# Kernel optimization log

Measured on AMD Instinct MI355X. Metric: run time of the kernel, lower is better.

The kernel has to match this reference:

```python
import jax, jax.numpy as jnp
import numpy as np

EMBED_DIM = 1024
NUM_HEADS = 16
HEAD_DIM = EMBED_DIM // NUM_HEADS


def setup_inputs() -> dict:
    key = jax.random.key(0)
    ks = jax.random.split(key, 9)
    B, S, E = 4, 2048, EMBED_DIM
    scale = 1.0 / np.sqrt(E)
    x = jax.random.normal(ks[0], (B, S, E), dtype=jnp.float32)
    # Linear layers: weight [E, E] (out, in) and bias [E], torch-style init scale
    Wq = jax.random.uniform(ks[1], (E, E), jnp.float32, -scale, scale)
    bq = jax.random.uniform(ks[2], (E,), jnp.float32, -scale, scale)
    Wk = jax.random.uniform(ks[3], (E, E), jnp.float32, -scale, scale)
    bk = jax.random.uniform(ks[4], (E,), jnp.float32, -scale, scale)
    Wv = jax.random.uniform(ks[5], (E, E), jnp.float32, -scale, scale)
    bv = jax.random.uniform(ks[6], (E,), jnp.float32, -scale, scale)
    Wo = jax.random.uniform(ks[7], (E, E), jnp.float32, -scale, scale)
    bo = jax.random.uniform(ks[8], (E,), jnp.float32, -scale, scale)
    return {"x": x, "Wq": Wq, "bq": bq, "Wk": Wk, "bk": bk,
            "Wv": Wv, "bv": bv, "Wo": Wo, "bo": bo}


def reference(x, Wq, bq, Wk, bk, Wv, bv, Wo, bo):
    B, S, E = x.shape
    H, D = NUM_HEADS, HEAD_DIM

    def proj(W, b):
        # torch Linear: x @ W.T + b ; reshape to [B, H, S, D]
        y = jnp.einsum('bse,fe->bsf', x, W) + b
        return y.reshape(B, S, H, D).transpose(0, 2, 1, 3)

    Q = proj(Wq, bq)
    K = proj(Wk, bk)
    V = proj(Wv, bv)
    scores = jnp.einsum('bhqd,bhkd->bhqk', Q, K) / jnp.sqrt(
        jnp.asarray(D, dtype=jnp.float32))
    attn = jax.nn.softmax(scores, axis=-1)
    out = jnp.einsum('bhqk,bhkd->bhqd', attn, V)
    out = out.transpose(0, 2, 1, 3).reshape(B, S, E)
    out = jnp.einsum('bse,fe->bsf', out, Wo) + bo
    return out
```

## Files before the change

### kernel.cpp

```cpp
#include <hip/hip_runtime.h>
#include <math.h>

#define SEQ 2048
#define EMB 1024
#define NH 16
#define HD 64
#define BATCH 4
#define MROWS (BATCH * SEQ)

typedef unsigned short u16;
typedef unsigned int u32;
typedef _Float16 f16;
using half8   = __attribute__((ext_vector_type(8))) f16;
using fp16x2  = __attribute__((ext_vector_type(2))) __fp16;
using vfloat4 = __attribute__((ext_vector_type(4))) float;

__device__ __forceinline__ u16 f2h(float f) {
    union { f16 h; u16 u; } x; x.h = (f16)f; return x.u;
}
__device__ __forceinline__ u32 pk2h(float a, float b) {
    union { fp16x2 h; u32 u; } x;
    x.h = __builtin_amdgcn_cvt_pkrtz(a, b);
    return x.u;
}
__device__ __forceinline__ float exp2v(float x) {
    float r; asm("v_exp_f32 %0, %1" : "=v"(r) : "v"(x)); return r;
}

__device__ __forceinline__ void gload16(const void* g, void* l) {
    __builtin_amdgcn_global_load_lds(
        (const __attribute__((address_space(1))) void*)g,
        (__attribute__((address_space(3))) void*)l, 16, 0, 0);
}

__global__ __launch_bounds__(256) void cvt5_kernel(
    const float* __restrict__ x,  const float* __restrict__ wq,
    const float* __restrict__ wk, const float* __restrict__ wv,
    const float* __restrict__ wo,
    uint2* __restrict__ xh, uint2* __restrict__ wqkv, uint2* __restrict__ woh)
{
    int gid = blockIdx.x * 256 + threadIdx.x;
    const float4* src; uint2* dst; int o;
    if (gid < (1 << 21)) {
        src = (const float4*)x; dst = xh; o = gid;
    } else {
        int g = gid - (1 << 21);
        int r = g >> 18;
        o = g & ((1 << 18) - 1);
        if      (r == 0) { src = (const float4*)wq; dst = wqkv; }
        else if (r == 1) { src = (const float4*)wk; dst = wqkv + (1 << 18); }
        else if (r == 2) { src = (const float4*)wv; dst = wqkv + (2 << 18); }
        else             { src = (const float4*)wo; dst = woh; }
    }
    float4 v = src[o];
    dst[o] = make_uint2(pk2h(v.x, v.y), pk2h(v.z, v.w));
}

__global__ __launch_bounds__(256) void gemm_qkv_kernel(
    const u16* __restrict__ A, const u16* __restrict__ Wqkv,
    const float* __restrict__ bq, const float* __restrict__ bk,
    const float* __restrict__ bv,
    u16* __restrict__ Qo, u16* __restrict__ Ko, u16* __restrict__ Vo,
    float sq)
{
    __shared__ char lds[32768];
    const int tid = threadIdx.x, wave = tid >> 6, lane = tid & 63;
    const int swz = (blockIdx.x & 7) * 192 + (blockIdx.x >> 3);
    const int bn = swz % 24, bm = swz / 24;
    const int mat = bn >> 3;
    const int wr = wave >> 1, wc = wave & 1;

    const int srow  = wave * 16 + (lane >> 2);
    const int sslot = lane & 3;
    const int ldso  = wave * 1024 + (lane << 4);
    const u16* Ab = A    + (size_t)bm * 128 * EMB;
    const u16* Wb = Wqkv + (size_t)bn * 128 * EMB;

    vfloat4 acc[4][4] = {};

#define QKV_STAGE(k0, bufi)                                                   \
    {                                                                         \
        char* Ad = lds + (bufi) * 16384;                                      \
        char* Bd = Ad + 8192;                                                 \
        _Pragma("unroll")                                                     \
        for (int i2 = 0; i2 < 2; ++i2) {                                      \
            int row = i2 * 64 + srow;                                         \
            int ko  = ((sslot ^ ((row >> 1) & 3)) << 3);                      \
            gload16(Ab + (size_t)row * EMB + (k0) + ko, Ad + i2 * 4096 + ldso); \
            gload16(Wb + (size_t)row * EMB + (k0) + ko, Bd + i2 * 4096 + ldso); \
        }                                                                     \
    }

    QKV_STAGE(0, 0);
    __syncthreads();

    for (int it = 0; it < EMB / 32; ++it) {
        const int cur = it & 1;
        if (it + 1 < EMB / 32) QKV_STAGE((it + 1) * 32, cur ^ 1);

        char* As = lds + cur * 16384;
        char* Bs = As + 8192;
        half8 af[4], bfr[4];
        #pragma unroll
        for (int m = 0; m < 4; ++m) {
            int r = wr * 64 + m * 16 + (lane & 15);
            af[m] = *(const half8*)(As + r * 64 + ((((lane >> 4) ^ ((r >> 1) & 3)) << 4)));
        }
        #pragma unroll
        for (int n = 0; n < 4; ++n) {
            int r = wc * 64 + n * 16 + (lane & 15);
            bfr[n] = *(const half8*)(Bs + r * 64 + ((((lane >> 4) ^ ((r >> 1) & 3)) << 4)));
        }
        #pragma unroll
        for (int m = 0; m < 4; ++m)
            #pragma unroll
            for (int n = 0; n < 4; ++n)
                acc[m][n] = __builtin_amdgcn_mfma_f32_16x16x32_f16(af[m], bfr[n], acc[m][n], 0, 0, 0);

        __syncthreads();
    }
#undef QKV_STAGE

    const float* bp = (mat == 0) ? bq : ((mat == 1) ? bk : bv);
    const float scale = (mat == 0) ? sq : 1.0f;
    u16* Co = (mat == 0) ? Qo : ((mat == 1) ? Ko : Vo);
    const int row0 = bm * 128 + wr * 64;
    const int col0 = (bn & 7) * 128 + wc * 64;

    #pragma unroll
    for (int n = 0; n < 4; ++n) {
        int col = col0 + n * 16 + (lane & 15);
        float bb = bp[col];
        int h = col >> 6, d = col & 63;
        if (mat != 2) {
            #pragma unroll
            for (int m = 0; m < 4; ++m)
                #pragma unroll
                for (int j = 0; j < 4; ++j) {
                    int row = row0 + m * 16 + (lane >> 4) * 4 + j;
                    int b = row >> 11, s = row & (SEQ - 1);
                    Co[(((size_t)(b * NH + h)) * SEQ + s) * HD + d] =
                        f2h((acc[m][n][j] + bb) * scale);
                }
        } else {
            #pragma unroll
            for (int m = 0; m < 4; ++m) {
                int row = row0 + m * 16 + (lane >> 4) * 4;
                int b = row >> 11, s = row & (SEQ - 1);
                u32 w0 = pk2h(acc[m][n][0] + bb, acc[m][n][1] + bb);
                u32 w1 = pk2h(acc[m][n][2] + bb, acc[m][n][3] + bb);
                *(uint2*)(Co + (((size_t)(b * NH + h)) * HD + d) * SEQ + s) =
                    make_uint2(w0, w1);
            }
        }
    }
}

__global__ __launch_bounds__(256) void gemm_f16_kernel(
    const u16* __restrict__ A, const u16* __restrict__ W,
    const float* __restrict__ bias, float* __restrict__ C)
{
    __shared__ char lds[32768];
    const int tid = threadIdx.x, wave = tid >> 6, lane = tid & 63;
    const int swz = (blockIdx.x & 7) * 64 + (blockIdx.x >> 3);
    const int bn = swz & 7, bm = swz >> 3;
    const int wr = wave >> 1, wc = wave & 1;

    const int srow  = wave * 16 + (lane >> 2);
    const int sslot = lane & 3;
    const int ldso  = wave * 1024 + (lane << 4);
    const u16* Ab = A + (size_t)bm * 128 * EMB;
    const u16* Wb = W + (size_t)bn * 128 * EMB;

    vfloat4 acc[4][4] = {};

#define F16_STAGE(k0, bufi)                                                   \
    {                                                                         \
        char* Ad = lds + (bufi) * 16384;                                      \
        char* Bd = Ad + 8192;                                                 \
        _Pragma("unroll")                                                     \
        for (int i2 = 0; i2 < 2; ++i2) {                                      \
            int row = i2 * 64 + srow;                                         \
            int ko  = ((sslot ^ ((row >> 1) & 3)) << 3);                      \
            gload16(Ab + (size_t)row * EMB + (k0) + ko, Ad + i2 * 4096 + ldso); \
            gload16(Wb + (size_t)row * EMB + (k0) + ko, Bd + i2 * 4096 + ldso); \
        }                                                                     \
    }

    F16_STAGE(0, 0);
    __syncthreads();

    for (int it = 0; it < EMB / 32; ++it) {
        const int cur = it & 1;
        if (it + 1 < EMB / 32) F16_STAGE((it + 1) * 32, cur ^ 1);

        char* As = lds + cur * 16384;
        char* Bs = As + 8192;
        half8 af[4], bfr[4];
        #pragma unroll
        for (int m = 0; m < 4; ++m) {
            int r = wr * 64 + m * 16 + (lane & 15);
            af[m] = *(const half8*)(As + r * 64 + ((((lane >> 4) ^ ((r >> 1) & 3)) << 4)));
        }
        #pragma unroll
        for (int n = 0; n < 4; ++n) {
            int r = wc * 64 + n * 16 + (lane & 15);
            bfr[n] = *(const half8*)(Bs + r * 64 + ((((lane >> 4) ^ ((r >> 1) & 3)) << 4)));
        }
        #pragma unroll
        for (int m = 0; m < 4; ++m)
            #pragma unroll
            for (int n = 0; n < 4; ++n)
                acc[m][n] = __builtin_amdgcn_mfma_f32_16x16x32_f16(af[m], bfr[n], acc[m][n], 0, 0, 0);

        __syncthreads();
    }
#undef F16_STAGE

    const int row0 = bm * 128 + wr * 64, col0 = bn * 128 + wc * 64;
    #pragma unroll
    for (int n = 0; n < 4; ++n) {
        int col = col0 + n * 16 + (lane & 15);
        float bb = bias[col];
        #pragma unroll
        for (int m = 0; m < 4; ++m)
            #pragma unroll
            for (int j = 0; j < 4; ++j) {
                int row = row0 + m * 16 + (lane >> 4) * 4 + j;
                C[(size_t)row * EMB + col] = acc[m][n][j] + bb;
            }
    }
}

__device__ __forceinline__ void stage_rows(const u16* g, int rstride, char* dst,
                                           int wave, int lane) {
    int r = wave * 8 + (lane >> 3), sl = lane & 7;
    #pragma unroll
    for (int i2 = 0; i2 < 2; ++i2) {
        int row = i2 * 32 + r;
        gload16(g + (size_t)row * rstride + ((sl ^ (row & 7)) << 3),
                dst + i2 * 4096 + wave * 1024 + (lane << 4));
    }
}

__global__ __launch_bounds__(256) void attn_kernel(
    const u16* __restrict__ Q, const u16* __restrict__ K,
    const u16* __restrict__ Vt, u16* __restrict__ O)
{
    __shared__ char lds[40960];
    char* QPs = lds;
    char* Kb0 = lds + 8192;
    char* Kb1 = lds + 16384;
    char* Vb0 = lds + 24576;
    char* Vb1 = lds + 32768;

    const int tid = threadIdx.x, wave = tid >> 6, lane = tid & 63;
    const int c = lane >> 4, li = lane & 15;

    const int swz = (blockIdx.x & 7) * 128 + (blockIdx.x >> 3);
    const int bh = swz >> 4;
    const int q0 = (swz & 15) << 7;

    const u16* Qg = Q  + ((size_t)bh * SEQ + q0) * HD;
    const u16* Kg = K  + (size_t)bh * SEQ * HD;
    const u16* Vg = Vt + (size_t)bh * HD * SEQ;

    const int srow8 = wave * 8 + (lane >> 3);
    const int ssl   = lane & 7;
    const int swzo  = ((ssl ^ (srow8 & 7)) << 3);
    const int ldo   = wave * 1024 + (lane << 4);
    const u16* kp = Kg + (size_t)srow8 * HD + swzo;
    const u16* vp = Vg + (size_t)srow8 * SEQ + swzo;

    stage_rows(Qg, HD, QPs, wave, lane);
    gload16(kp, Kb0 + ldo);  gload16(kp + 32 * HD, Kb0 + 4096 + ldo);
    gload16(vp, Vb0 + ldo);  gload16(vp + 32 * SEQ, Vb0 + 4096 + ldo);
    kp += 64 * HD;  vp += 64;
    __syncthreads();

    half8 qf[2][2];
    const int q = wave * 16 + li;
    #pragma unroll
    for (int cc = 0; cc < 2; ++cc)
        qf[0][cc] = *(const half8*)(QPs + q * 128 + (((4 * cc + c) ^ (q & 7)) << 4));
    __syncthreads();
    stage_rows(Qg + (size_t)64 * HD, HD, QPs, wave, lane);
    __syncthreads();
    #pragma unroll
    for (int cc = 0; cc < 2; ++cc)
        qf[1][cc] = *(const half8*)(QPs + q * 128 + (((4 * cc + c) ^ (q & 7)) << 4));

    const half8 ones8 = {1, 1, 1, 1, 1, 1, 1, 1};
    char* Pw = QPs + wave * 2048;
    vfloat4 o0[4] = {}, o1[4] = {};
    vfloat4 l0 = {}, l1 = {};

    for (int kt = 0; kt < SEQ / 64; ++kt) {
        char* Kc = (kt & 1) ? Kb1 : Kb0;
        char* Vc = (kt & 1) ? Vb1 : Vb0;
        if (kt < SEQ / 64 - 1) {
            char* kd = (kt & 1) ? Kb0 : Kb1;
            char* vd = (kt & 1) ? Vb0 : Vb1;
            gload16(kp, kd + ldo);  gload16(kp + 32 * HD, kd + 4096 + ldo);
            gload16(vp, vd + ldo);  gload16(vp + 32 * SEQ, vd + 4096 + ldo);
            kp += 64 * HD;  vp += 64;
        }

        vfloat4 s0[4] = {}, s1[4] = {};
        __builtin_amdgcn_s_setprio(1);
        #pragma unroll
        for (int n = 0; n < 4; ++n) {
            int key = 16 * n + li;
            #pragma unroll
            for (int cc = 0; cc < 2; ++cc) {
                half8 kb = *(const half8*)(Kc + key * 128 + (((4 * cc + c) ^ (li & 7)) << 4));
                s0[n] = __builtin_amdgcn_mfma_f32_16x16x32_f16(kb, qf[0][cc], s0[n], 0, 0, 0);
                s1[n] = __builtin_amdgcn_mfma_f32_16x16x32_f16(kb, qf[1][cc], s1[n], 0, 0, 0);
            }
        }
        __builtin_amdgcn_s_setprio(0);

        #pragma unroll
        for (int n = 0; n < 4; ++n)
            #pragma unroll
            for (int j = 0; j < 4; ++j) {
                s0[n][j] = exp2v(s0[n][j]);
                s1[n][j] = exp2v(s1[n][j]);
            }

        half8 pf0[2], pf1[2];
        #pragma unroll
        for (int n = 0; n < 4; ++n) {
            u32 w0 = pk2h(s0[n][0], s0[n][1]);
            u32 w1 = pk2h(s0[n][2], s0[n][3]);
            *(uint2*)(Pw + li * 128 + (((2 * n + (c >> 1)) ^ (li & 7)) << 4) + ((c & 1) << 3))
                = make_uint2(w0, w1);
        }
        #pragma unroll
        for (int cc = 0; cc < 2; ++cc)
            pf0[cc] = *(const half8*)(Pw + li * 128 + (((4 * cc + c) ^ (li & 7)) << 4));
        #pragma unroll
        for (int n = 0; n < 4; ++n) {
            u32 w0 = pk2h(s1[n][0], s1[n][1]);
            u32 w1 = pk2h(s1[n][2], s1[n][3]);
            *(uint2*)(Pw + li * 128 + (((2 * n + (c >> 1)) ^ (li & 7)) << 4) + ((c & 1) << 3))
                = make_uint2(w0, w1);
        }
        #pragma unroll
        for (int cc = 0; cc < 2; ++cc)
            pf1[cc] = *(const half8*)(Pw + li * 128 + (((4 * cc + c) ^ (li & 7)) << 4));

        __builtin_amdgcn_s_setprio(1);
        #pragma unroll
        for (int n = 0; n < 4; ++n) {
            int r = 16 * n + li;
            #pragma unroll
            for (int cc = 0; cc < 2; ++cc) {
                half8 vf = *(const half8*)(Vc + r * 128 + (((4 * cc + c) ^ (li & 7)) << 4));
                o0[n] = __builtin_amdgcn_mfma_f32_16x16x32_f16(vf, pf0[cc], o0[n], 0, 0, 0);
                o1[n] = __builtin_amdgcn_mfma_f32_16x16x32_f16(vf, pf1[cc], o1[n], 0, 0, 0);
            }
        }
        #pragma unroll
        for (int cc = 0; cc < 2; ++cc) {
            l0 = __builtin_amdgcn_mfma_f32_16x16x32_f16(ones8, pf0[cc], l0, 0, 0, 0);
            l1 = __builtin_amdgcn_mfma_f32_16x16x32_f16(ones8, pf1[cc], l1, 0, 0, 0);
        }
        __builtin_amdgcn_s_setprio(0);

        __syncthreads();
    }

    const int b = bh >> 4, h = bh & 15;
    const size_t r0 = ((size_t)b * SEQ + q0 + wave * 16 + li) * EMB + h * 64;
    const size_t r1 = ((size_t)b * SEQ + q0 + 64 + wave * 16 + li) * EMB + h * 64;
    float i0 = 1.0f / l0[0];
    float i1 = 1.0f / l1[0];
    #pragma unroll
    for (int n = 0; n < 4; ++n) {
        *(uint2*)(O + r0 + 16 * n + 4 * c) =
            make_uint2(pk2h(o0[n][0] * i0, o0[n][1] * i0),
                       pk2h(o0[n][2] * i0, o0[n][3] * i0));
        *(uint2*)(O + r1 + 16 * n + 4 * c) =
            make_uint2(pk2h(o1[n][0] * i1, o1[n][1] * i1),
                       pk2h(o1[n][2] * i1, o1[n][3] * i1));
    }
}

extern "C" void kernel_launch(void* const* d_in, const int* in_sizes, int n_in,
                              void* d_out, int out_size, void* d_ws, size_t ws_size,
                              hipStream_t stream) {
    const float* x  = (const float*)d_in[0];
    const float* Wq = (const float*)d_in[1];
    const float* bq = (const float*)d_in[2];
    const float* Wk = (const float*)d_in[3];
    const float* bk = (const float*)d_in[4];
    const float* Wv = (const float*)d_in[5];
    const float* bv = (const float*)d_in[6];
    const float* Wo = (const float*)d_in[7];
    const float* bo = (const float*)d_in[8];
    float* out = (float*)d_out;

    char* ws = (char*)d_ws;
    u16* xh   = (u16*)(ws);
    u16* Qh   = (u16*)(ws + ((size_t)16 << 20));
    u16* Kh   = (u16*)(ws + ((size_t)32 << 20));
    u16* Vh   = (u16*)(ws + ((size_t)48 << 20));
    u16* Ah   = (u16*)(ws + ((size_t)64 << 20));
    u16* Wqkv = (u16*)(ws + ((size_t)80 << 20));
    u16* Woh  = (u16*)(ws + ((size_t)88 << 20));

    const int nCvt = (1 << 21) + (1 << 20);

    cvt5_kernel<<<nCvt / 256, 256, 0, stream>>>(
        x, Wq, Wk, Wv, Wo, (uint2*)xh, (uint2*)Wqkv, (uint2*)Woh);

    const float SCALE_Q = 0.125f * 1.4426950408889634f;
    gemm_qkv_kernel<<<dim3(3 * EMB / 128 * MROWS / 128), 256, 0, stream>>>(
        xh, Wqkv, bq, bk, bv, Qh, Kh, Vh, SCALE_Q);

    attn_kernel<<<dim3(SEQ / 128 * BATCH * NH), 256, 0, stream>>>(Qh, Kh, Vh, Ah);

    gemm_f16_kernel<<<dim3(EMB / 128 * MROWS / 128), 256, 0, stream>>>(Ah, Woh, bo, out);
}
```

Before: 216.7 us.

## Read K and V fragments directly from global memory, dropping LDS double buffering

The attention kernel stops staging K and V tiles into double-buffered shared memory. MFMA operand fragments are now loaded straight from global memory (through the caches), and LDS is cut to 8 KB for Q and P only. The per-iteration block barrier is removed. This cuts LDS footprint and sync overhead, which may raise occupancy, but every wave now issues its own uncoalesced global loads with no prefetch, so the MFMAs may stall on memory latency.

```diff
diff --git a/kernel.cpp b/kernel.cpp
--- a/kernel.cpp
+++ b/kernel.cpp
@@ -247,12 +247,7 @@
     const u16* __restrict__ Q, const u16* __restrict__ K,
     const u16* __restrict__ Vt, u16* __restrict__ O)
 {
-    __shared__ char lds[40960];
-    char* QPs = lds;
-    char* Kb0 = lds + 8192;
-    char* Kb1 = lds + 16384;
-    char* Vb0 = lds + 24576;
-    char* Vb1 = lds + 32768;
+    __shared__ char lds[8192];
 
     const int tid = threadIdx.x, wave = tid >> 6, lane = tid & 63;
     const int c = lane >> 4, li = lane & 15;
@@ -265,60 +260,43 @@
     const u16* Kg = K  + (size_t)bh * SEQ * HD;
     const u16* Vg = Vt + (size_t)bh * HD * SEQ;
 
-    const int srow8 = wave * 8 + (lane >> 3);
-    const int ssl   = lane & 7;
-    const int swzo  = ((ssl ^ (srow8 & 7)) << 3);
-    const int ldo   = wave * 1024 + (lane << 4);
-    const u16* kp = Kg + (size_t)srow8 * HD + swzo;
-    const u16* vp = Vg + (size_t)srow8 * SEQ + swzo;
-
-    stage_rows(Qg, HD, QPs, wave, lane);
-    gload16(kp, Kb0 + ldo);  gload16(kp + 32 * HD, Kb0 + 4096 + ldo);
-    gload16(vp, Vb0 + ldo);  gload16(vp + 32 * SEQ, Vb0 + 4096 + ldo);
-    kp += 64 * HD;  vp += 64;
+    stage_rows(Qg, HD, lds, wave, lane);
     __syncthreads();
-
     half8 qf[2][2];
     const int q = wave * 16 + li;
     #pragma unroll
     for (int cc = 0; cc < 2; ++cc)
-        qf[0][cc] = *(const half8*)(QPs + q * 128 + (((4 * cc + c) ^ (q & 7)) << 4));
+        qf[0][cc] = *(const half8*)(lds + q * 128 + (((4 * cc + c) ^ (q & 7)) << 4));
     __syncthreads();
-    stage_rows(Qg + (size_t)64 * HD, HD, QPs, wave, lane);
+    stage_rows(Qg + (size_t)64 * HD, HD, lds, wave, lane);
     __syncthreads();
     #pragma unroll
     for (int cc = 0; cc < 2; ++cc)
-        qf[1][cc] = *(const half8*)(QPs + q * 128 + (((4 * cc + c) ^ (q & 7)) << 4));
+        qf[1][cc] = *(const half8*)(lds + q * 128 + (((4 * cc + c) ^ (q & 7)) << 4));
 
     const half8 ones8 = {1, 1, 1, 1, 1, 1, 1, 1};
-    char* Pw = QPs + wave * 2048;
+    char* Pw = lds + wave * 2048;
     vfloat4 o0[4] = {}, o1[4] = {};
     vfloat4 l0 = {}, l1 = {};
 
+    const u16* kp = Kg + li * HD + 8 * c;
+    const u16* vpn[4];
+    #pragma unroll
+    for (int n = 0; n < 4; ++n) vpn[n] = Vg + (size_t)(16 * n + li) * SEQ + 8 * c;
+
     for (int kt = 0; kt < SEQ / 64; ++kt) {
-        char* Kc = (kt & 1) ? Kb1 : Kb0;
-        char* Vc = (kt & 1) ? Vb1 : Vb0;
-        if (kt < SEQ / 64 - 1) {
-            char* kd = (kt & 1) ? Kb0 : Kb1;
-            char* vd = (kt & 1) ? Vb0 : Vb1;
-            gload16(kp, kd + ldo);  gload16(kp + 32 * HD, kd + 4096 + ldo);
-            gload16(vp, vd + ldo);  gload16(vp + 32 * SEQ, vd + 4096 + ldo);
-            kp += 64 * HD;  vp += 64;
-        }
-
         vfloat4 s0[4] = {}, s1[4] = {};
         __builtin_amdgcn_s_setprio(1);
         #pragma unroll
-        for (int n = 0; n < 4; ++n) {
-            int key = 16 * n + li;
+        for (int n = 0; n < 4; ++n)
             #pragma unroll
             for (int cc = 0; cc < 2; ++cc) {
-                half8 kb = *(const half8*)(Kc + key * 128 + (((4 * cc + c) ^ (li & 7)) << 4));
+                half8 kb = *(const half8*)(kp + n * 1024 + cc * 32);
                 s0[n] = __builtin_amdgcn_mfma_f32_16x16x32_f16(kb, qf[0][cc], s0[n], 0, 0, 0);
                 s1[n] = __builtin_amdgcn_mfma_f32_16x16x32_f16(kb, qf[1][cc], s1[n], 0, 0, 0);
             }
-        }
         __builtin_amdgcn_s_setprio(0);
+        kp += 4096;
 
         #pragma unroll
         for (int n = 0; n < 4; ++n)
@@ -352,23 +330,21 @@
 
         __builtin_amdgcn_s_setprio(1);
         #pragma unroll
-        for (int n = 0; n < 4; ++n) {
-            int r = 16 * n + li;
+        for (int n = 0; n < 4; ++n)
             #pragma unroll
             for (int cc = 0; cc < 2; ++cc) {
-                half8 vf = *(const half8*)(Vc + r * 128 + (((4 * cc + c) ^ (li & 7)) << 4));
+                half8 vf = *(const half8*)(vpn[n] + cc * 32);
                 o0[n] = __builtin_amdgcn_mfma_f32_16x16x32_f16(vf, pf0[cc], o0[n], 0, 0, 0);
                 o1[n] = __builtin_amdgcn_mfma_f32_16x16x32_f16(vf, pf1[cc], o1[n], 0, 0, 0);
             }
-        }
         #pragma unroll
         for (int cc = 0; cc < 2; ++cc) {
             l0 = __builtin_amdgcn_mfma_f32_16x16x32_f16(ones8, pf0[cc], l0, 0, 0, 0);
             l1 = __builtin_amdgcn_mfma_f32_16x16x32_f16(ones8, pf1[cc], l1, 0, 0, 0);
         }
         __builtin_amdgcn_s_setprio(0);
-
-        __syncthreads();
+        #pragma unroll
+        for (int n = 0; n < 4; ++n) vpn[n] += 64;
     }
 
     const int b = bh >> 4, h = bh & 15;
```

After: 402.2 us. 1.86x slower.
